# Optimization experiments

Hardware: AMD Instinct MI355X
Metric: run time of the kernel (lower is better)

The kernel has to match this reference:

```python
import jax, jax.numpy as jnp
import numpy as np

BLOCK = 16
H = 16
KV = 4
HPG = H // KV
DH = 64
SCALE = 1.0 / np.sqrt(DH).astype(np.float32)


def setup_inputs() -> dict:
    key = jax.random.key(0)
    ks = jax.random.split(key, 7)
    B, Ldec, Lenc, D = 2, 8192, 4096, 1024
    s = 1.0 / np.sqrt(D).astype(np.float32)
    return {
        "hidden_states": jax.random.normal(ks[0], (B, Ldec, D), jnp.float32),
        "encoder_hidden_states": jax.random.normal(ks[1], (B, Lenc, D), jnp.float32),
        "attention_mask": jax.random.randint(ks[2], (B, Lenc), 0, 2, jnp.int32),
        "Wq": jax.random.normal(ks[3], (D, H * DH), jnp.float32) * s,
        "Wk": jax.random.normal(ks[4], (D, KV * DH), jnp.float32) * s,
        "Wv": jax.random.normal(ks[5], (D, KV * DH), jnp.float32) * s,
        "Wo": jax.random.normal(ks[6], (H * DH, D), jnp.float32) * s,
    }


def reference(hidden_states, encoder_hidden_states, attention_mask, Wq, Wk, Wv, Wo):
    B, Ldec, D = hidden_states.shape
    Lenc = encoder_hidden_states.shape[1]
    pad = (BLOCK - Ldec % BLOCK) % BLOCK
    x = jnp.pad(hidden_states, ((0, 0), (0, pad), (0, 0))) if pad else hidden_states
    nb = (Ldec + pad) // BLOCK
    # mean-pool decoder tokens into blocks: [B, nb, D]
    pooled = x.reshape(B, nb, BLOCK, D).mean(axis=2)
    # projections; GQA: group q heads by kv head (repeat_interleave order)
    q = (pooled @ Wq).reshape(B, nb, KV, HPG, DH)          # [B, nb, KV, HPG, DH]
    k = (encoder_hidden_states @ Wk).reshape(B, Lenc, KV, DH)
    v = (encoder_hidden_states @ Wv).reshape(B, Lenc, KV, DH)
    scores = jnp.einsum("bngqd,blgd->bgqnl", q, k) * SCALE  # [B, KV, HPG, nb, Lenc]
    mask = (attention_mask == 0)[:, None, None, None, :]
    scores = jnp.where(mask, jnp.float32(-1e9), scores)
    attn = jax.nn.softmax(scores, axis=-1)
    out = jnp.einsum("bgqnl,blgd->bngqd", attn, v)          # [B, nb, KV, HPG, DH]
    out = out.reshape(B, nb, H * DH) @ Wo                   # [B, nb, D]
    # broadcast block output back to token level
    unpooled = jnp.broadcast_to(out[:, :, None, :], (B, nb, BLOCK, D)).reshape(B, nb * BLOCK, D)
    return unpooled[:, :Ldec, :]
```

## Files before the change

kernel.cpp:

```cpp
#include <hip/hip_runtime.h>


typedef unsigned short u16;
typedef __attribute__((ext_vector_type(8))) __bf16 bf16x8;
typedef __attribute__((ext_vector_type(4))) float f32x4;
typedef __attribute__((ext_vector_type(4))) _Float16 f16x4;

static __device__ __forceinline__ u16 f2bf(float f) {
    unsigned int u = __float_as_uint(f);
    u = (u + 0x7fffu + ((u >> 16) & 1u)) >> 16;
    return (u16)u;
}
static __device__ __forceinline__ void gload16(const u16* g, u16* l) {
    __builtin_amdgcn_global_load_lds(
        (const __attribute__((address_space(1))) void*)g,
        (__attribute__((address_space(3))) void*)l, 16, 0, 0);
}

__global__ __launch_bounds__(256) void prep_all(const float* __restrict__ enc,
                                                const float* __restrict__ hid,
                                                const int* __restrict__ mask,
                                                const float* __restrict__ Wq,
                                                const float* __restrict__ Wk,
                                                const float* __restrict__ Wv,
                                                const float* __restrict__ Wo,
                                                u16* __restrict__ encb,
                                                u16* __restrict__ poolb,
                                                u16* __restrict__ mh,
                                                u16* __restrict__ Wq_t,
                                                u16* __restrict__ Wkv_t,
                                                u16* __restrict__ Wo_t) {
    int bid = blockIdx.x;
    if (bid < 2560) {
        const float* in; u16* out; int N, nbx, rowoff;
        if (bid < 1024)      { in = Wq; out = Wq_t;  N = 1024; nbx = 32; rowoff = 0; }
        else if (bid < 2048) { in = Wo; out = Wo_t;  N = 1024; nbx = 32; rowoff = 0; bid -= 1024; }
        else if (bid < 2304) { in = Wk; out = Wkv_t; N = 256;  nbx = 8;  rowoff = 0; bid -= 2048; }
        else                 { in = Wv; out = Wkv_t; N = 256;  nbx = 8;  rowoff = 256; bid -= 2304; }
        const int n0 = (bid % nbx) * 32, k0 = (bid / nbx) * 32;
        __shared__ float t[32][33];
        const int tx = threadIdx.x & 31, ty = threadIdx.x >> 5;
#pragma unroll
        for (int i = 0; i < 4; ++i)
            t[ty + 8 * i][tx] = in[(size_t)(k0 + ty + 8 * i) * N + n0 + tx];
        __syncthreads();
#pragma unroll
        for (int i = 0; i < 4; ++i)
            out[(size_t)(rowoff + n0 + ty + 8 * i) * 1024 + k0 + tx] = f2bf(t[tx][ty + 8 * i]);
    } else if (bid < 10752) {
        const int tid = (bid - 2560) * 256 + threadIdx.x;
        float4 v = ((const float4*)enc)[tid];
        ushort4 o;
        o.x = f2bf(v.x); o.y = f2bf(v.y); o.z = f2bf(v.z); o.w = f2bf(v.w);
        ((ushort4*)encb)[tid] = o;
    } else if (bid < 11776) {
        const int tid = (bid - 10752) * 256 + threadIdx.x;
        const int c4 = tid & 255;
        const int row = tid >> 8;
        const float4* src = (const float4*)(hid + (size_t)row * 16 * 1024) + c4;
        float4 a = src[0];
#pragma unroll
        for (int t = 1; t < 16; ++t) {
            float4 b = src[(size_t)t * 256];
            a.x += b.x; a.y += b.y; a.z += b.z; a.w += b.w;
        }
        ushort4 o;
        o.x = f2bf(a.x * 0.0625f); o.y = f2bf(a.y * 0.0625f);
        o.z = f2bf(a.z * 0.0625f); o.w = f2bf(a.w * 0.0625f);
        *(ushort4*)(poolb + (size_t)row * 1024 + c4 * 4) = o;
    } else {
#pragma unroll
        for (int k = 0; k < 32; ++k) {
            const int i = threadIdx.x + 256 * k;
            mh[i] = mask[i] ? (u16)0x3C00 : (u16)0;
        }
    }
}

template <int MODE>
static __device__ __forceinline__ void gemm_core(const u16* __restrict__ A,
                                                 const u16* __restrict__ Bt,
                                                 const int* __restrict__ maskp,
                                                 u16* __restrict__ outK,
                                                 u16* __restrict__ outV,
                                                 float* __restrict__ out_f,
                                                 int m0, int n0) {
    __shared__ __align__(16) u16 sAB[2 * 64 * 72];
    u16* sA = sAB;
    u16* sB = sAB + 64 * 64;
    const int t = threadIdx.x;
    const int w = t >> 6, lane = t & 63, quad = lane >> 4, r16 = lane & 15;
    const int row8 = lane >> 3, seg = lane & 7;

    f32x4 acc[4];
#pragma unroll
    for (int i = 0; i < 4; ++i) acc[i] = (f32x4){0.f, 0.f, 0.f, 0.f};

    for (int kt = 0; kt < 16; ++kt) {
        const int k0 = kt * 64;
        __syncthreads();
#pragma unroll
        for (int j = 0; j < 2; ++j) {
            const int ra = w * 16 + j * 8;
            gload16(A + (size_t)(m0 + ra + row8) * 1024 + k0 + seg * 8, sA + ra * 64);
            gload16(Bt + (size_t)(n0 + ra + row8) * 1024 + k0 + seg * 8, sB + ra * 64);
        }
        __syncthreads();
#pragma unroll
        for (int kk = 0; kk < 2; ++kk) {
            const bf16x8 af = *(const bf16x8*)(sA + (16 * w + r16) * 64 + kk * 32 + quad * 8);
#pragma unroll
            for (int nt = 0; nt < 4; ++nt) {
                const bf16x8 bfv = *(const bf16x8*)(sB + (nt * 16 + r16) * 64 + kk * 32 + quad * 8);
                acc[nt] = __builtin_amdgcn_mfma_f32_16x16x32_bf16(af, bfv, acc[nt], 0, 0, 0);
            }
        }
    }

    if (MODE == 0) {
#pragma unroll
        for (int nt = 0; nt < 4; ++nt)
#pragma unroll
            for (int r = 0; r < 4; ++r) {
                const int m = m0 + 16 * w + quad * 4 + r;
                const int c = n0 + nt * 16 + r16;
                const int b = m >> 9, nq = m & 511, g = c >> 8, qh = (c >> 6) & 3, d = c & 63;
                outK[((((size_t)(b * 4 + g) * 4 + qh) * 512 + nq) << 6) + d] =
                    f2bf(acc[nt][r] * 0.180336880f);
            }
    } else if (MODE == 4) {
        const bool isV = (n0 >= 256);
        const int g = (isV ? (n0 - 256) : n0) >> 6;
        const int b = m0 >> 12, l0 = m0 & 4095;
        u16* sT = sAB;
        __syncthreads();
        if (isV) {
            float mfl[4];
#pragma unroll
            for (int r = 0; r < 4; ++r)
                mfl[r] = maskp[b * 4096 + l0 + 16 * w + quad * 4 + r] ? 1.f : 0.f;
#pragma unroll
            for (int nt = 0; nt < 4; ++nt)
#pragma unroll
                for (int r = 0; r < 4; ++r) {
                    const int ml = 16 * w + quad * 4 + r, cl = nt * 16 + r16;
                    union { _Float16 h; u16 u; } cv;
                    cv.h = (_Float16)(acc[nt][r] * mfl[r]);
                    sT[cl * 72 + ml] = cv.u;
                }
        } else {
#pragma unroll
            for (int nt = 0; nt < 4; ++nt)
#pragma unroll
                for (int r = 0; r < 4; ++r) {
                    const int ml = 16 * w + quad * 4 + r, cl = nt * 16 + r16;
                    sT[ml * 72 + cl] = f2bf(acc[nt][r]);
                }
        }
        __syncthreads();
#pragma unroll
        for (int p = 0; p < 2; ++p) {
            const int idx = t + 256 * p, rr = idx >> 3, ch = idx & 7;
            const int4 v = *(const int4*)(sT + rr * 72 + ch * 8);
            if (isV)
                *(int4*)(outV + ((size_t)(b * 4 + g) * 64 + rr) * 4096 + l0 + ch * 8) = v;
            else
                *(int4*)(outK + (((size_t)(b * 4 + g) * 4096 + l0 + rr) << 6) + ch * 8) = v;
        }
    } else {
#pragma unroll
        for (int nt = 0; nt < 4; ++nt)
#pragma unroll
            for (int r = 0; r < 4; ++r) {
                const int m = m0 + 16 * w + quad * 4 + r;
                const int c = n0 + nt * 16 + r16;
                out_f[(size_t)m * 1024 + c] = acc[nt][r];
            }
    }
}

__global__ __launch_bounds__(256) void gemm_qkv(const u16* __restrict__ poolb,
                                                const u16* __restrict__ encb,
                                                const u16* __restrict__ Wq_t,
                                                const u16* __restrict__ Wkv_t,
                                                const int* __restrict__ maskp,
                                                u16* __restrict__ Qa,
                                                u16* __restrict__ Ka,
                                                u16* __restrict__ Va) {
    const int bx = blockIdx.x;
    if (bx < 1024) {
        gemm_core<4>(encb, Wkv_t, maskp, Ka, Va, nullptr, (bx >> 3) * 64, (bx & 7) * 64);
    } else {
        const int b = bx - 1024;
        gemm_core<0>(poolb, Wq_t, nullptr, Qa, nullptr, nullptr, (b >> 4) * 64, (b & 15) * 64);
    }
}

__global__ __launch_bounds__(256) void gemm_o(const u16* __restrict__ attn,
                                              const u16* __restrict__ Wo_t,
                                              float* __restrict__ blk) {
    gemm_core<3>(attn, Wo_t, nullptr, nullptr, nullptr, blk, (blockIdx.x >> 4) * 64,
                 (blockIdx.x & 15) * 64);
}

__global__ __launch_bounds__(256, 4) void flash_attn(const u16* __restrict__ Qa,
                                                     const u16* __restrict__ Ka,
                                                     const u16* __restrict__ Vt,
                                                     const u16* __restrict__ mh,
                                                     float* __restrict__ Opart,
                                                     float* __restrict__ mlpart) {
    const int bx = blockIdx.x;
    const int s16 = bx & 31, rr = bx >> 5;
    const int split = rr & 3, gb = rr >> 2;
    const int g = gb & 3, b = gb >> 2;
    __shared__ __align__(16) u16 sK[64 * 72];
    __shared__ __align__(16) u16 sV[64 * 68];
    const int t = threadIdx.x;
    const int qh = t >> 6, lane = t & 63, quad = lane >> 4, r16 = lane & 15;

    bf16x8 aq[2];
    {
        const size_t qbase = ((((size_t)(b * 4 + g) * 4 + qh) * 512) + s16 * 16 + r16) * 64;
#pragma unroll
        for (int kk = 0; kk < 2; ++kk)
            aq[kk] = *(const bf16x8*)(Qa + qbase + kk * 32 + quad * 8);
    }
    const u16* Kg = Ka + (size_t)(b * 4 + g) * 4096 * 64 + (size_t)split * 1024 * 64;
    const u16* Vg = Vt + (size_t)(b * 4 + g) * 64 * 4096 + split * 1024;
    const u16* mb = mh + b * 4096 + split * 1024 + quad * 4;

    f32x4 o[4], lacc;
#pragma unroll
    for (int i = 0; i < 4; ++i) o[i] = (f32x4){0.f, 0.f, 0.f, 0.f};
    lacc = (f32x4){0.f, 0.f, 0.f, 0.f};

    for (int tile = 0; tile < 16; ++tile) {
        const int l0 = tile * 64;
        __syncthreads();
#pragma unroll
        for (int p = 0; p < 2; ++p) {
            const int idx = t + 256 * p, row = idx >> 3, seg = idx & 7;
            *(int4*)(sK + row * 72 + seg * 8) =
                *(const int4*)(Kg + (size_t)(l0 + row) * 64 + seg * 8);
            *(int4*)(sV + row * 68 + seg * 8) =
                *(const int4*)(Vg + (size_t)row * 4096 + l0 + seg * 8);
        }
        __syncthreads();

        f32x4 st[4];
#pragma unroll
        for (int nt = 0; nt < 4; ++nt) st[nt] = (f32x4){0.f, 0.f, 0.f, 0.f};
#pragma unroll
        for (int kk = 0; kk < 2; ++kk)
#pragma unroll
            for (int nt = 0; nt < 4; ++nt) {
                const bf16x8 ka = *(const bf16x8*)(sK + (nt * 16 + r16) * 72 + kk * 32 + quad * 8);
                st[nt] = __builtin_amdgcn_mfma_f32_16x16x32_bf16(ka, aq[kk], st[nt], 0, 0, 0);
            }

#pragma unroll
        for (int nt = 0; nt < 4; ++nt) {
            f16x4 pa;
#pragma unroll
            for (int j = 0; j < 4; ++j)
                pa[j] = (_Float16)__builtin_amdgcn_exp2f(st[nt][j]);
            const f16x4 bvm = *(const f16x4*)(mb + l0 + nt * 16);
            lacc = __builtin_amdgcn_mfma_f32_16x16x16f16(pa, bvm, lacc, 0, 0, 0);
#pragma unroll
            for (int dt = 0; dt < 4; ++dt) {
                const f16x4 bv = *(const f16x4*)(sV + (dt * 16 + r16) * 68 + nt * 16 + quad * 4);
                o[dt] = __builtin_amdgcn_mfma_f32_16x16x16f16(pa, bv, o[dt], 0, 0, 0);
            }
        }
    }

    const size_t pbase = ((size_t)bx * 4 + qh) * 1024;
#pragma unroll
    for (int dt = 0; dt < 4; ++dt)
#pragma unroll
        for (int r = 0; r < 4; ++r)
            Opart[pbase + (size_t)(quad * 4 + r) * 64 + dt * 16 + r16] = o[dt][r];
    if (r16 == 0) {
#pragma unroll
        for (int r = 0; r < 4; ++r)
            mlpart[((size_t)bx * 4 + qh) * 16 + quad * 4 + r] = lacc[r];
    }
}

__global__ __launch_bounds__(256) void flash_combine(const float* __restrict__ Opart,
                                                     const float* __restrict__ mlpart,
                                                     u16* __restrict__ attnout) {
    const int bx = blockIdx.x;
    const int s16 = bx & 31, h = bx >> 5;
    const int qh = h & 3, g = (h >> 2) & 3, b = h >> 4;
    const int t = threadIdx.x;
    const int q = t >> 4, dg = t & 15;
    float4 a = make_float4(0.f, 0.f, 0.f, 0.f);
    float L = 0.f;
#pragma unroll
    for (int s = 0; s < 4; ++s) {
        const size_t part = (((size_t)((b * 4 + g) * 4 + s) * 32 + s16) * 4 + qh);
        const float4 v = *(const float4*)(Opart + part * 1024 + q * 64 + dg * 4);
        a.x += v.x; a.y += v.y; a.z += v.z; a.w += v.w;
        L += mlpart[part * 16 + q];
    }
    const float invL = 1.f / L;
    ushort4 ov;
    ov.x = f2bf(a.x * invL); ov.y = f2bf(a.y * invL);
    ov.z = f2bf(a.z * invL); ov.w = f2bf(a.w * invL);
    *(ushort4*)(attnout + ((size_t)b * 512 + s16 * 16 + q) * 1024 +
                (g * 4 + qh) * 64 + dg * 4) = ov;
}

__global__ __launch_bounds__(256) void bcast_out(const float* __restrict__ blockout,
                                                 float* __restrict__ out) {
    const int tid = blockIdx.x * 256 + threadIdx.x;
    const int c4 = tid & 255;
    const int row = tid >> 8;
    const int b = row >> 13, l = row & 8191;
    ((float4*)out)[tid] = ((const float4*)blockout)[((size_t)(b * 512 + (l >> 4)) << 8) + c4];
}

extern "C" void kernel_launch(void* const* d_in, const int* in_sizes, int n_in,
                              void* d_out, int out_size, void* d_ws, size_t ws_size,
                              hipStream_t stream) {
    const float* hid  = (const float*)d_in[0];
    const float* enc  = (const float*)d_in[1];
    const int*   mask = (const int*)d_in[2];
    const float* Wq   = (const float*)d_in[3];
    const float* Wk   = (const float*)d_in[4];
    const float* Wv   = (const float*)d_in[5];
    const float* Wo   = (const float*)d_in[6];
    float* out = (float*)d_out;

    char* ws = (char*)d_ws;
    size_t off = 0;
    auto alloc = [&](size_t bytes) -> char* {
        char* p = ws + off;
        off += (bytes + 255) & ~(size_t)255;
        return p;
    };
    u16* Wq_t  = (u16*)alloc((size_t)1024 * 1024 * 2);
    u16* Wkv_t = (u16*)alloc((size_t)512 * 1024 * 2);
    u16* Wo_t  = (u16*)alloc((size_t)1024 * 1024 * 2);
    u16* encb  = (u16*)alloc((size_t)8192 * 1024 * 2);
    u16* poolb = (u16*)alloc((size_t)1024 * 1024 * 2);
    u16* Qa    = (u16*)alloc((size_t)1024 * 1024 * 2);
    u16* Ka    = (u16*)alloc((size_t)8 * 4096 * 64 * 2);
    u16* Va    = (u16*)alloc((size_t)8 * 4096 * 64 * 2);
    u16* attn  = (u16*)alloc((size_t)1024 * 1024 * 2);
    float* blk = (float*)alloc((size_t)1024 * 1024 * 4);
    u16* mh    = (u16*)alloc((size_t)8192 * 2);
    float* Opart  = (float*)encb;
    float* mlpart = (float*)poolb;

    prep_all<<<11777, 256, 0, stream>>>(enc, hid, mask, Wq, Wk, Wv, Wo,
                                        encb, poolb, mh, Wq_t, Wkv_t, Wo_t);
    gemm_qkv<<<1280, 256, 0, stream>>>(poolb, encb, Wq_t, Wkv_t, mask, Qa, Ka, Va);
    flash_attn<<<1024, 256, 0, stream>>>(Qa, Ka, Va, mh, Opart, mlpart);
    flash_combine<<<1024, 256, 0, stream>>>(Opart, mlpart, attn);
    gemm_o<<<256, 256, 0, stream>>>(attn, Wo_t, blk);
    bcast_out<<<16384, 256, 0, stream>>>(blk, out);
}
```

Baseline: 253.2 us.

## Split-K output GEMM with reduction fused into broadcast, coarsen enc conversion

The output projection GEMM is split along K into four partial products, giving four times as many blocks. The partials go into the reused encoder buffer. The broadcast kernel now sums the four partials and writes each pooled row to its 16 token rows, with one thread per pooled element instead of per token. The encoder bf16 conversion processes four vectors per thread to reduce block count. The cost is extra partial-sum traffic in exchange for better GPU occupancy in the small GEMM and fewer redundant reads in the broadcast.

Measured after the change: 248.5 us. About the same (-1.9%).

```diff
diff --git a/kernel.cpp b/kernel.cpp
--- a/kernel.cpp
+++ b/kernel.cpp
@@ -47,14 +47,20 @@
 #pragma unroll
         for (int i = 0; i < 4; ++i)
             out[(size_t)(rowoff + n0 + ty + 8 * i) * 1024 + k0 + tx] = f2bf(t[tx][ty + 8 * i]);
-    } else if (bid < 10752) {
-        const int tid = (bid - 2560) * 256 + threadIdx.x;
-        float4 v = ((const float4*)enc)[tid];
-        ushort4 o;
-        o.x = f2bf(v.x); o.y = f2bf(v.y); o.z = f2bf(v.z); o.w = f2bf(v.w);
-        ((ushort4*)encb)[tid] = o;
-    } else if (bid < 11776) {
-        const int tid = (bid - 10752) * 256 + threadIdx.x;
+    } else if (bid < 4608) {
+        const int base = (bid - 2560) * 1024 + threadIdx.x;
+        float4 v[4];
+#pragma unroll
+        for (int j = 0; j < 4; ++j) v[j] = ((const float4*)enc)[base + j * 256];
+#pragma unroll
+        for (int j = 0; j < 4; ++j) {
+            ushort4 o;
+            o.x = f2bf(v[j].x); o.y = f2bf(v[j].y);
+            o.z = f2bf(v[j].z); o.w = f2bf(v[j].w);
+            ((ushort4*)encb)[base + j * 256] = o;
+        }
+    } else if (bid < 5632) {
+        const int tid = (bid - 4608) * 256 + threadIdx.x;
         const int c4 = tid & 255;
         const int row = tid >> 8;
         const float4* src = (const float4*)(hid + (size_t)row * 16 * 1024) + c4;
@@ -84,7 +90,7 @@
                                                  u16* __restrict__ outK,
                                                  u16* __restrict__ outV,
                                                  float* __restrict__ out_f,
-                                                 int m0, int n0) {
+                                                 int m0, int n0, int kt0, int nkt) {
     __shared__ __align__(16) u16 sAB[2 * 64 * 72];
     u16* sA = sAB;
     u16* sB = sAB + 64 * 64;
@@ -96,7 +102,7 @@
 #pragma unroll
     for (int i = 0; i < 4; ++i) acc[i] = (f32x4){0.f, 0.f, 0.f, 0.f};
 
-    for (int kt = 0; kt < 16; ++kt) {
+    for (int kt = kt0; kt < kt0 + nkt; ++kt) {
         const int k0 = kt * 64;
         __syncthreads();
 #pragma unroll
@@ -189,18 +195,20 @@
                                                 u16* __restrict__ Va) {
     const int bx = blockIdx.x;
     if (bx < 1024) {
-        gemm_core<4>(encb, Wkv_t, maskp, Ka, Va, nullptr, (bx >> 3) * 64, (bx & 7) * 64);
+        gemm_core<4>(encb, Wkv_t, maskp, Ka, Va, nullptr, (bx >> 3) * 64, (bx & 7) * 64, 0, 16);
     } else {
         const int b = bx - 1024;
-        gemm_core<0>(poolb, Wq_t, nullptr, Qa, nullptr, nullptr, (b >> 4) * 64, (b & 15) * 64);
+        gemm_core<0>(poolb, Wq_t, nullptr, Qa, nullptr, nullptr, (b >> 4) * 64, (b & 15) * 64, 0, 16);
     }
 }
 
 __global__ __launch_bounds__(256) void gemm_o(const u16* __restrict__ attn,
                                               const u16* __restrict__ Wo_t,
-                                              float* __restrict__ blk) {
-    gemm_core<3>(attn, Wo_t, nullptr, nullptr, nullptr, blk, (blockIdx.x >> 4) * 64,
-                 (blockIdx.x & 15) * 64);
+                                              float* __restrict__ blkpart) {
+    const int bx = blockIdx.x;
+    const int s = bx >> 8, m0 = ((bx >> 4) & 15) * 64, n0 = (bx & 15) * 64;
+    gemm_core<3>(attn, Wo_t, nullptr, nullptr, nullptr,
+                 blkpart + ((size_t)s << 20), m0, n0, s * 4, 4);
 }
 
 __global__ __launch_bounds__(256, 4) void flash_attn(const u16* __restrict__ Qa,
@@ -312,13 +320,22 @@
                 (g * 4 + qh) * 64 + dg * 4) = ov;
 }
 
-__global__ __launch_bounds__(256) void bcast_out(const float* __restrict__ blockout,
+__global__ __launch_bounds__(256) void bcast_out(const float* __restrict__ blkpart,
                                                  float* __restrict__ out) {
     const int tid = blockIdx.x * 256 + threadIdx.x;
     const int c4 = tid & 255;
     const int row = tid >> 8;
-    const int b = row >> 13, l = row & 8191;
-    ((float4*)out)[tid] = ((const float4*)blockout)[((size_t)(b * 512 + (l >> 4)) << 8) + c4];
+    float4 a = make_float4(0.f, 0.f, 0.f, 0.f);
+#pragma unroll
+    for (int s = 0; s < 4; ++s) {
+        const float4 v = ((const float4*)blkpart)[(s << 18) + (row << 8) + c4];
+        a.x += v.x; a.y += v.y; a.z += v.z; a.w += v.w;
+    }
+    const int b = row >> 9, n = row & 511;
+    float4* dst = (float4*)out + (((size_t)b * 8192 + n * 16) << 8) + c4;
+#pragma unroll
+    for (int rep = 0; rep < 16; ++rep)
+        dst[(size_t)rep << 8] = a;
 }
 
 extern "C" void kernel_launch(void* const* d_in, const int* in_sizes, int n_in,
@@ -349,16 +366,16 @@
     u16* Ka    = (u16*)alloc((size_t)8 * 4096 * 64 * 2);
     u16* Va    = (u16*)alloc((size_t)8 * 4096 * 64 * 2);
     u16* attn  = (u16*)alloc((size_t)1024 * 1024 * 2);
-    float* blk = (float*)alloc((size_t)1024 * 1024 * 4);
     u16* mh    = (u16*)alloc((size_t)8192 * 2);
-    float* Opart  = (float*)encb;
-    float* mlpart = (float*)poolb;
-
-    prep_all<<<11777, 256, 0, stream>>>(enc, hid, mask, Wq, Wk, Wv, Wo,
-                                        encb, poolb, mh, Wq_t, Wkv_t, Wo_t);
+    float* Opart   = (float*)encb;
+    float* blkpart = (float*)encb;
+    float* mlpart  = (float*)poolb;
+
+    prep_all<<<5633, 256, 0, stream>>>(enc, hid, mask, Wq, Wk, Wv, Wo,
+                                       encb, poolb, mh, Wq_t, Wkv_t, Wo_t);
     gemm_qkv<<<1280, 256, 0, stream>>>(poolb, encb, Wq_t, Wkv_t, mask, Qa, Ka, Va);
     flash_attn<<<1024, 256, 0, stream>>>(Qa, Ka, Va, mh, Opart, mlpart);
     flash_combine<<<1024, 256, 0, stream>>>(Opart, mlpart, attn);
-    gemm_o<<<256, 256, 0, stream>>>(attn, Wo_t, blk);
-    bcast_out<<<16384, 256, 0, stream>>>(blk, out);
-}
+    gemm_o<<<1024, 256, 0, stream>>>(attn, Wo_t, blkpart);
+    bcast_out<<<1024, 256, 0, stream>>>(blkpart, out);
+}
```
